# Kernel optimization log

Hardware: AMD Instinct MI355X
Metric: run time of the kernel (lower is better)

The kernel has to match this reference:

```python
import jax, jax.numpy as jnp
import numpy as np
from jax import lax

NEG_INF = -jnp.inf

def _conv_same(x, w, b):
    # x: [B,C,H,W], w: [O,C,5,5], padding=2 (SAME for k=5)
    y = lax.conv_general_dilated(x, w, (1, 1), [(2, 2), (2, 2)],
                                 dimension_numbers=('NCHW', 'OIHW', 'NCHW'))
    return y + b[None, :, None, None]

def _maxpool3(x):
    # kernel=3, stride=3, VALID: 28x28 -> 9x9
    return lax.reduce_window(x, -jnp.inf, lax.max, (1, 1, 3, 3), (1, 1, 3, 3), 'VALID')

def _trunk(x, w1, b1, w2, b2):
    # x: [B,1,28,28] -> [B, 16*9*9]
    h = jax.nn.relu(_conv_same(x, w1, b1))
    h = jax.nn.relu(_conv_same(h, w2, b2))
    h = _maxpool3(h)
    return h.reshape(h.shape[0], -1)

def _iterator(state, c_w1, c_b1, c_w2, c_b2, c_wl, c_bl):
    # state: [B,28,28]
    B = state.shape[0]
    xd = state[:, None]                                   # [B,1,28,28]
    feat = _trunk(xd, c_w1, c_b1, c_w2, c_b2)             # [B,1296]
    w = jnp.tanh(feat @ c_wl + c_bl).reshape(B, 1, 13, 13)  # per-sample kernels [O=B,I=1,13,13]
    xp = jnp.pad(xd, ((0, 0), (0, 0), (6, 6), (6, 6)), constant_values=-1.0)  # [B,1,40,40]
    xg = xp.reshape(1, B, 40, 40)
    yg = lax.conv_general_dilated(xg, w, (1, 1), 'VALID',
                                  feature_group_count=B,
                                  dimension_numbers=('NCHW', 'OIHW', 'NCHW'))  # [1,B,28,28]
    return yg.reshape(B, 28, 28)

def setup_inputs() -> dict:
    key = jax.random.key(0)
    ks = jax.random.split(key, 13)
    s = 0.05
    B = 1024
    inp = {
        'x': jax.random.normal(ks[0], (B, 28, 28), jnp.float32),
        # determine_n params
        'n_w1': jax.random.normal(ks[1], (8, 1, 5, 5), jnp.float32) * s,
        'n_b1': jnp.zeros((8,), jnp.float32),
        'n_w2': jax.random.normal(ks[2], (16, 8, 5, 5), jnp.float32) * s,
        'n_b2': jnp.zeros((16,), jnp.float32),
        'n_wl': jax.random.normal(ks[3], (16 * 9 * 9, 10), jnp.float32) * s,
        'n_bl': jnp.zeros((10,), jnp.float32),
        # determine_conv params
        'c_w1': jax.random.normal(ks[4], (8, 1, 5, 5), jnp.float32) * s,
        'c_b1': jnp.zeros((8,), jnp.float32),
        'c_w2': jax.random.normal(ks[5], (16, 8, 5, 5), jnp.float32) * s,
        'c_b2': jnp.zeros((16,), jnp.float32),
        'c_wl': jax.random.normal(ks[6], (16 * 9 * 9, 13 * 13), jnp.float32) * s,
        'c_bl': jnp.zeros((13 * 13,), jnp.float32),
    }
    return inp

def reference(x, n_w1, n_b1, n_w2, n_b2, n_wl, n_bl,
              c_w1, c_b1, c_w2, c_b2, c_wl, c_bl):
    B = x.shape[0]
    xd = x.reshape(B, 1, 28, 28)
    # determine_n: soft natural number over {0..9}
    num = jnp.tanh(_trunk(xd, n_w1, n_b1, n_w2, n_b2) @ n_wl + n_bl)  # [B,10]
    # TmIter: weighted sum of iterates r_0..r_9, r_{k+1} = iterator(r_k)
    r = x
    out = num[:, 0, None, None] * r
    for k in range(1, 10):  # fixed 9-step unroll (num encodes naturals 0..9)
        r = _iterator(r, c_w1, c_b1, c_w2, c_b2, c_wl, c_bl)
        out = out + num[:, k, None, None] * r
    return out.reshape(-1, 28, 28)
```

## Files before the change

### kernel.cpp

```cpp
#include <hip/hip_runtime.h>
#include <math.h>

#define RP40S 44
#define H1W   31

struct SharedBufs {
    float rp40[40*RP40S];
    float h1p[8*28*H1W];
    float pbuf[1296];
    float wker[169];
    float num_s[10];
    int   next;
};

template<int OUT>
__device__ __forceinline__ void fc_tanh(const float* __restrict__ Wg,
                                        const float* __restrict__ bg,
                                        const float* __restrict__ p,
                                        float* __restrict__ dst, int tid)
{
    if (tid < OUT) {
        float a[8];
        #pragma unroll
        for (int u = 0; u < 8; ++u) a[u] = 0.f;
        #pragma unroll 4
        for (int i0 = 0; i0 < 1296; i0 += 8) {
            #pragma unroll
            for (int u = 0; u < 8; ++u)
                a[u] = fmaf(p[i0+u], Wg[(i0+u)*OUT + tid], a[u]);
        }
        float s = ((a[0]+a[1])+(a[2]+a[3])) + ((a[4]+a[5])+(a[6]+a[7])) + bg[tid];
        dst[tid] = tanhf(s);
    }
}

#define C2_LOADROW(dst, YY) {                                                  \
    int rr_ = crow0 + (YY); rr_ = rr_ < 2 ? 2 : (rr_ > 29 ? 29 : rr_);         \
    const float* hp_ = plane + (rr_ - 2)*H1W;                                  \
    _Pragma("unroll") for (int j = 0; j < 13; ++j) dst[j] = hp_[j]; }

#define C2_FMAROW(src, YY)                                                     \
    if ((unsigned)(crow0 + (YY) - 2) <= 27u) {                                 \
      _Pragma("unroll") for (int t = 0; t < 3; ++t) {                          \
        const int ky_ = (YY) - t;                                              \
        if (ky_ >= 0 && ky_ <= 4) {                                            \
          _Pragma("unroll") for (int kx = 0; kx < 5; ++kx) {                   \
            const float w_ = wreg[ky_*5+kx];                                   \
            _Pragma("unroll") for (int u = 0; u < 9; ++u)                      \
              acc[t*9+u] = fmaf(w_, src[u+kx], acc[t*9+u]); } } } }

__device__ __forceinline__ void trunk_pass(SharedBufs& sb, int tid,
                                           const float* __restrict__ w1g,
                                           const float* __restrict__ b1g,
                                           const float* __restrict__ w2g,
                                           const float* __restrict__ b2g)
{
    if (tid < 224) {
        const int c = tid & 7;
        const int y = tid >> 3;
        float wreg[25];
        #pragma unroll
        for (int t = 0; t < 25; ++t) wreg[t] = w1g[c*25 + t];
        float csR[5];
        float S_all = 0.f, SR = 0.f;
        #pragma unroll
        for (int kx = 0; kx < 5; ++kx) {
            float a = wreg[kx] + wreg[5+kx] + wreg[10+kx] + wreg[15+kx] + wreg[20+kx];
            float ex = 0.f;
            if (y == 0)       ex = wreg[kx] + wreg[5+kx];
            else if (y == 1)  ex = wreg[kx];
            if (y == 26)      ex += wreg[20+kx];
            else if (y == 27) ex += wreg[15+kx] + wreg[20+kx];
            csR[kx] = a - ex;
            S_all += a; SR += csR[kx];
        }
        const float corrI = S_all - SR;
        const float bias  = b1g[c];
        float acc[28];
        #pragma unroll
        for (int x = 0; x < 28; ++x) acc[x] = bias + corrI;
        acc[0]  += csR[0] + csR[1];
        acc[1]  += csR[0];
        acc[26] += csR[4];
        acc[27] += csR[3] + csR[4];
        #pragma unroll
        for (int ky = 0; ky < 5; ++ky) {
            const float4* rr = (const float4*)&sb.rp40[(y+4+ky)*RP40S + 4];
            float rv[32];
            #pragma unroll
            for (int q = 0; q < 8; ++q) {
                float4 t = rr[q];
                rv[q*4+0]=t.x; rv[q*4+1]=t.y; rv[q*4+2]=t.z; rv[q*4+3]=t.w;
            }
            #pragma unroll
            for (int kx = 0; kx < 5; ++kx) {
                const float w = wreg[ky*5+kx];
                #pragma unroll
                for (int x = 0; x < 28; ++x) acc[x] = fmaf(w, rv[x+kx], acc[x]);
            }
        }
        float* hp = &sb.h1p[(c*28 + y)*H1W + 2];
        #pragma unroll
        for (int x = 0; x < 28; ++x) hp[x] = fmaxf(acc[x], 0.f);
    }
    __syncthreads();

    if (tid < 240) {
        const int c    = tid / 15;
        const int rem  = tid % 15;
        const int pyg  = rem / 3;
        const int pxg  = rem % 3;
        const int col0 = pxg * 9;
        const float bias = b2g[c];
        #pragma unroll 1
        for (int h = 0; h < 2; ++h) {
            const int py = pyg*2 + h;
            if (py >= 9) break;
            const int crow0 = py * 3;
            float acc[27];
            #pragma unroll
            for (int i = 0; i < 27; ++i) acc[i] = bias;
            for (int ic = 0; ic < 8; ++ic) {
                float wreg[25];
                const float* wsrc = &w2g[(c*8+ic)*25];
                #pragma unroll
                for (int t = 0; t < 25; ++t) wreg[t] = wsrc[t];
                const float* plane = &sb.h1p[ic*28*H1W + col0];
                float ra[13], rb[13];
                C2_LOADROW(ra, 0)
                C2_LOADROW(rb, 1)  C2_FMAROW(ra, 0)
                C2_LOADROW(ra, 2)  C2_FMAROW(rb, 1)
                C2_LOADROW(rb, 3)  C2_FMAROW(ra, 2)
                C2_LOADROW(ra, 4)  C2_FMAROW(rb, 3)
                C2_LOADROW(rb, 5)  C2_FMAROW(ra, 4)
                C2_LOADROW(ra, 6)  C2_FMAROW(rb, 5)
                                   C2_FMAROW(ra, 6)
            }
            #pragma unroll
            for (int pxi = 0; pxi < 3; ++pxi) {
                float m = acc[pxi*3];
                #pragma unroll
                for (int dy = 0; dy < 3; ++dy)
                    #pragma unroll
                    for (int dx = 0; dx < 3; ++dx)
                        m = fmaxf(m, acc[dy*9 + pxi*3 + dx]);
                sb.pbuf[c*81 + py*9 + pxg*3 + pxi] = fmaxf(m, 0.f);
            }
        }
    }
    __syncthreads();
}

__device__ __forceinline__ void depthwise13_regs(SharedBufs& sb, int y, int x0,
                                                 float& a0, float& a1,
                                                 float& a2, float& a3)
{
    a0=0.f; a1=0.f; a2=0.f; a3=0.f;
    #pragma unroll 1
    for (int ky = 0; ky < 13; ++ky) {
        const float4* rr = (const float4*)&sb.rp40[(y+ky)*RP40S + x0];
        float rv[16];
        #pragma unroll
        for (int q = 0; q < 4; ++q) {
            float4 t = rr[q];
            rv[q*4+0]=t.x; rv[q*4+1]=t.y; rv[q*4+2]=t.z; rv[q*4+3]=t.w;
        }
        const float* wr = &sb.wker[ky*13];
        #pragma unroll
        for (int kx = 0; kx < 13; ++kx) {
            const float w = wr[kx];
            a0 = fmaf(w, rv[kx+0], a0);
            a1 = fmaf(w, rv[kx+1], a1);
            a2 = fmaf(w, rv[kx+2], a2);
            a3 = fmaf(w, rv[kx+3], a3);
        }
    }
}

__global__ __launch_bounds__(256) __attribute__((amdgpu_num_vgpr(128)))
void modeld_fused(const float* __restrict__ x,
                  const float* __restrict__ n_w1, const float* __restrict__ n_b1,
                  const float* __restrict__ n_w2, const float* __restrict__ n_b2,
                  const float* __restrict__ n_wl, const float* __restrict__ n_bl,
                  const float* __restrict__ c_w1, const float* __restrict__ c_b1,
                  const float* __restrict__ c_w2, const float* __restrict__ c_b2,
                  const float* __restrict__ c_wl, const float* __restrict__ c_bl,
                  float* __restrict__ out,
                  int* __restrict__ counter, int B)
{
    __shared__ SharedBufs sb;
    const int tid = threadIdx.x;
    const int dy  = tid / 7;
    const int dx0 = (tid % 7) * 4;

    for (int i = tid; i < 40*RP40S;   i += 256) sb.rp40[i] = -1.f;
    for (int i = tid; i < 8*28*H1W;   i += 256) sb.h1p[i]  = 0.f;

    while (true) {
        if (tid == 0) sb.next = atomicAdd(counter, 1);
        __syncthreads();
        const int b = sb.next;
        if (b >= B) break;

        float cur[4] = {0.f, 0.f, 0.f, 0.f};
        if (tid < 196) {
            const float4 t = *(const float4*)&x[b*784 + dy*28 + dx0];
            cur[0]=t.x; cur[1]=t.y; cur[2]=t.z; cur[3]=t.w;
            float* rp = &sb.rp40[(dy+6)*RP40S + dx0 + 6];
            rp[0]=t.x; rp[1]=t.y; rp[2]=t.z; rp[3]=t.w;
        }
        __syncthreads();

        trunk_pass(sb, tid, n_w1, n_b1, n_w2, n_b2);
        fc_tanh<10>(n_wl, n_bl, sb.pbuf, sb.num_s, tid);
        __syncthreads();

        float o[4];
        {
            const float n0 = sb.num_s[0];
            #pragma unroll
            for (int q = 0; q < 4; ++q) o[q] = n0 * cur[q];
        }

        for (int k = 1; k <= 9; ++k) {
            trunk_pass(sb, tid, c_w1, c_b1, c_w2, c_b2);
            fc_tanh<169>(c_wl, c_bl, sb.pbuf, sb.wker, tid);
            __syncthreads();
            float a0, a1, a2, a3;
            if (tid < 196) depthwise13_regs(sb, dy, dx0, a0, a1, a2, a3);
            __syncthreads();
            if (tid < 196) {
                const float nk = sb.num_s[k];
                o[0] = fmaf(nk, a0, o[0]);
                o[1] = fmaf(nk, a1, o[1]);
                o[2] = fmaf(nk, a2, o[2]);
                o[3] = fmaf(nk, a3, o[3]);
                float* rp = &sb.rp40[(dy+6)*RP40S + dx0 + 6];
                rp[0]=a0; rp[1]=a1; rp[2]=a2; rp[3]=a3;
            }
            __syncthreads();
        }

        if (tid < 196)
            *(float4*)&out[b*784 + dy*28 + dx0] = make_float4(o[0], o[1], o[2], o[3]);
    }
}

extern "C" void kernel_launch(void* const* d_in, const int* in_sizes, int n_in,
                              void* d_out, int out_size, void* d_ws, size_t ws_size,
                              hipStream_t stream)
{
    const float* x    = (const float*)d_in[0];
    const float* n_w1 = (const float*)d_in[1];
    const float* n_b1 = (const float*)d_in[2];
    const float* n_w2 = (const float*)d_in[3];
    const float* n_b2 = (const float*)d_in[4];
    const float* n_wl = (const float*)d_in[5];
    const float* n_bl = (const float*)d_in[6];
    const float* c_w1 = (const float*)d_in[7];
    const float* c_b1 = (const float*)d_in[8];
    const float* c_w2 = (const float*)d_in[9];
    const float* c_b2 = (const float*)d_in[10];
    const float* c_wl = (const float*)d_in[11];
    const float* c_bl = (const float*)d_in[12];
    float* out = (float*)d_out;

    const int B = in_sizes[0] / 784;
    hipMemsetAsync(d_ws, 0, sizeof(int), stream);
    const int grid = B < 1024 ? B : 1024;
    hipLaunchKernelGGL(modeld_fused, dim3(grid), dim3(256), 0, stream,
                       x, n_w1, n_b1, n_w2, n_b2, n_wl, n_bl,
                       c_w1, c_b1, c_w2, c_b2, c_wl, c_bl, out,
                       (int*)d_ws, B);
}
```

Measured before the change: 1.342 ms.

## Register-block conv2 over channel pairs and vectorize shared-memory loads

Conv2 is reorganized so each thread computes two output channels for one pooled row, reusing each loaded input row for both channels. That replaces the earlier loop where each thread handled two pooled rows of one channel. The h1p stride is widened to allow float2 stores and loads, and the FC layer reads features as float4. The VGPR budget is raised to 168, which lowers occupancy, and the persistent grid is cut to 768 blocks to match.

```diff
diff --git a/kernel.cpp b/kernel.cpp
--- a/kernel.cpp
+++ b/kernel.cpp
@@ -2,7 +2,7 @@
 #include <math.h>
 
 #define RP40S 44
-#define H1W   31
+#define H1W   34
 
 struct SharedBufs {
     float rp40[40*RP40S];
@@ -25,29 +25,21 @@
         for (int u = 0; u < 8; ++u) a[u] = 0.f;
         #pragma unroll 4
         for (int i0 = 0; i0 < 1296; i0 += 8) {
-            #pragma unroll
-            for (int u = 0; u < 8; ++u)
-                a[u] = fmaf(p[i0+u], Wg[(i0+u)*OUT + tid], a[u]);
+            const float4 p0 = *(const float4*)&p[i0];
+            const float4 p1 = *(const float4*)&p[i0+4];
+            a[0] = fmaf(p0.x, Wg[(i0+0)*OUT + tid], a[0]);
+            a[1] = fmaf(p0.y, Wg[(i0+1)*OUT + tid], a[1]);
+            a[2] = fmaf(p0.z, Wg[(i0+2)*OUT + tid], a[2]);
+            a[3] = fmaf(p0.w, Wg[(i0+3)*OUT + tid], a[3]);
+            a[4] = fmaf(p1.x, Wg[(i0+4)*OUT + tid], a[4]);
+            a[5] = fmaf(p1.y, Wg[(i0+5)*OUT + tid], a[5]);
+            a[6] = fmaf(p1.z, Wg[(i0+6)*OUT + tid], a[6]);
+            a[7] = fmaf(p1.w, Wg[(i0+7)*OUT + tid], a[7]);
         }
         float s = ((a[0]+a[1])+(a[2]+a[3])) + ((a[4]+a[5])+(a[6]+a[7])) + bg[tid];
         dst[tid] = tanhf(s);
     }
 }
-
-#define C2_LOADROW(dst, YY) {                                                  \
-    int rr_ = crow0 + (YY); rr_ = rr_ < 2 ? 2 : (rr_ > 29 ? 29 : rr_);         \
-    const float* hp_ = plane + (rr_ - 2)*H1W;                                  \
-    _Pragma("unroll") for (int j = 0; j < 13; ++j) dst[j] = hp_[j]; }
-
-#define C2_FMAROW(src, YY)                                                     \
-    if ((unsigned)(crow0 + (YY) - 2) <= 27u) {                                 \
-      _Pragma("unroll") for (int t = 0; t < 3; ++t) {                          \
-        const int ky_ = (YY) - t;                                              \
-        if (ky_ >= 0 && ky_ <= 4) {                                            \
-          _Pragma("unroll") for (int kx = 0; kx < 5; ++kx) {                   \
-            const float w_ = wreg[ky_*5+kx];                                   \
-            _Pragma("unroll") for (int u = 0; u < 9; ++u)                      \
-              acc[t*9+u] = fmaf(w_, src[u+kx], acc[t*9+u]); } } } }
 
 __device__ __forceinline__ void trunk_pass(SharedBufs& sb, int tid,
                                            const float* __restrict__ w1g,
@@ -99,52 +91,83 @@
                 for (int x = 0; x < 28; ++x) acc[x] = fmaf(w, rv[x+kx], acc[x]);
             }
         }
-        float* hp = &sb.h1p[(c*28 + y)*H1W + 2];
-        #pragma unroll
-        for (int x = 0; x < 28; ++x) hp[x] = fmaxf(acc[x], 0.f);
+        float2* hp = (float2*)&sb.h1p[(c*28 + y)*H1W + 2];
+        #pragma unroll
+        for (int x = 0; x < 14; ++x)
+            hp[x] = make_float2(fmaxf(acc[2*x], 0.f), fmaxf(acc[2*x+1], 0.f));
     }
     __syncthreads();
 
     if (tid < 240) {
-        const int c    = tid / 15;
-        const int rem  = tid % 15;
-        const int pyg  = rem / 3;
-        const int pxg  = rem % 3;
-        const int col0 = pxg * 9;
-        const float bias = b2g[c];
-        #pragma unroll 1
-        for (int h = 0; h < 2; ++h) {
-            const int py = pyg*2 + h;
-            if (py >= 9) break;
+        const int cpair = tid / 30;
+        const int sp    = tid % 30;
+        const int h     = sp / 15;
+        const int rem   = sp % 15;
+        const int pyg   = rem / 3;
+        const int pxg   = rem % 3;
+        const int py    = pyg*2 + h;
+        if (py < 9) {
+            const int cA = cpair*2, cB = cA + 1;
+            const int colw = (pxg*9) & ~1;
+            const bool oddc = (pxg == 1);
             const int crow0 = py * 3;
-            float acc[27];
-            #pragma unroll
-            for (int i = 0; i < 27; ++i) acc[i] = bias;
+            float accA[27], accB[27];
+            {
+                const float bA = b2g[cA], bB = b2g[cB];
+                #pragma unroll
+                for (int i = 0; i < 27; ++i) { accA[i] = bA; accB[i] = bB; }
+            }
             for (int ic = 0; ic < 8; ++ic) {
-                float wreg[25];
-                const float* wsrc = &w2g[(c*8+ic)*25];
-                #pragma unroll
-                for (int t = 0; t < 25; ++t) wreg[t] = wsrc[t];
-                const float* plane = &sb.h1p[ic*28*H1W + col0];
-                float ra[13], rb[13];
-                C2_LOADROW(ra, 0)
-                C2_LOADROW(rb, 1)  C2_FMAROW(ra, 0)
-                C2_LOADROW(ra, 2)  C2_FMAROW(rb, 1)
-                C2_LOADROW(rb, 3)  C2_FMAROW(ra, 2)
-                C2_LOADROW(ra, 4)  C2_FMAROW(rb, 3)
-                C2_LOADROW(rb, 5)  C2_FMAROW(ra, 4)
-                C2_LOADROW(ra, 6)  C2_FMAROW(rb, 5)
-                                   C2_FMAROW(ra, 6)
+                float wA[25], wB[25];
+                {
+                    const float* sA = &w2g[(cA*8+ic)*25];
+                    const float* sB = &w2g[(cB*8+ic)*25];
+                    #pragma unroll
+                    for (int t = 0; t < 25; ++t) { wA[t] = sA[t]; wB[t] = sB[t]; }
+                }
+                #pragma unroll
+                for (int yy = 0; yy < 7; ++yy) {
+                    const int rr = crow0 + yy;
+                    if ((unsigned)(rr - 2) > 27u) continue;
+                    const float2* h2 = (const float2*)&sb.h1p[(ic*28 + (rr-2))*H1W + colw];
+                    float f[14];
+                    #pragma unroll
+                    for (int q = 0; q < 7; ++q) {
+                        float2 t = h2[q];
+                        f[2*q] = t.x; f[2*q+1] = t.y;
+                    }
+                    float rowv[13];
+                    #pragma unroll
+                    for (int j = 0; j < 13; ++j) rowv[j] = oddc ? f[j+1] : f[j];
+                    #pragma unroll
+                    for (int t = 0; t < 3; ++t) {
+                        const int ky = yy - t;
+                        if (ky < 0 || ky > 4) continue;
+                        #pragma unroll
+                        for (int kx = 0; kx < 5; ++kx) {
+                            const float wa = wA[ky*5+kx];
+                            const float wb = wB[ky*5+kx];
+                            #pragma unroll
+                            for (int u = 0; u < 9; ++u) {
+                                accA[t*9+u] = fmaf(wa, rowv[u+kx], accA[t*9+u]);
+                                accB[t*9+u] = fmaf(wb, rowv[u+kx], accB[t*9+u]);
+                            }
+                        }
+                    }
+                }
             }
             #pragma unroll
             for (int pxi = 0; pxi < 3; ++pxi) {
-                float m = acc[pxi*3];
+                float mA = accA[pxi*3], mB = accB[pxi*3];
                 #pragma unroll
                 for (int dy = 0; dy < 3; ++dy)
                     #pragma unroll
-                    for (int dx = 0; dx < 3; ++dx)
-                        m = fmaxf(m, acc[dy*9 + pxi*3 + dx]);
-                sb.pbuf[c*81 + py*9 + pxg*3 + pxi] = fmaxf(m, 0.f);
+                    for (int dx = 0; dx < 3; ++dx) {
+                        mA = fmaxf(mA, accA[dy*9 + pxi*3 + dx]);
+                        mB = fmaxf(mB, accB[dy*9 + pxi*3 + dx]);
+                    }
+                sb.pbuf[cA*81 + py*9 + pxg*3 + pxi] = fmaxf(mA, 0.f);
+                sb.pbuf[cB*81 + py*9 + pxg*3 + pxi] = fmaxf(mB, 0.f);
             }
         }
     }
@@ -177,7 +200,7 @@
     }
 }
 
-__global__ __launch_bounds__(256) __attribute__((amdgpu_num_vgpr(128)))
+__global__ __launch_bounds__(256) __attribute__((amdgpu_num_vgpr(168)))
 void modeld_fused(const float* __restrict__ x,
                   const float* __restrict__ n_w1, const float* __restrict__ n_b1,
                   const float* __restrict__ n_w2, const float* __restrict__ n_b2,
@@ -267,7 +290,7 @@
 
     const int B = in_sizes[0] / 784;
     hipMemsetAsync(d_ws, 0, sizeof(int), stream);
-    const int grid = B < 1024 ? B : 1024;
+    const int grid = B < 768 ? B : 768;
     hipLaunchKernelGGL(modeld_fused, dim3(grid), dim3(256), 0, stream,
                        x, n_w1, n_b1, n_w2, n_b2, n_wl, n_bl,
                        c_w1, c_b1, c_w2, c_b2, c_wl, c_bl, out,
```

After: 2.513 ms. 87.2% more time.

## Double-buffer iterate state to drop a barrier; vectorize FC loads, retune VGPRs and grid

Applied to the files above, without the earlier changes.

Splits the padded state buffer into two ping-pong copies, so the depthwise conv reads the current buffer and writes the next. This removes one __syncthreads per iteration. The FC loop now reads its pooled features as float4, the VGPR cap rises from 128 to 168, and the persistent grid shrinks from 1024 to 768 blocks. The larger shared footprint and register budget may lower occupancy, which the smaller grid partly anticipates.

```diff
diff --git a/kernel.cpp b/kernel.cpp
--- a/kernel.cpp
+++ b/kernel.cpp
@@ -5,7 +5,7 @@
 #define H1W   31
 
 struct SharedBufs {
-    float rp40[40*RP40S];
+    float rp40[2][40*RP40S];
     float h1p[8*28*H1W];
     float pbuf[1296];
     float wker[169];
@@ -25,9 +25,16 @@
         for (int u = 0; u < 8; ++u) a[u] = 0.f;
         #pragma unroll 4
         for (int i0 = 0; i0 < 1296; i0 += 8) {
-            #pragma unroll
-            for (int u = 0; u < 8; ++u)
-                a[u] = fmaf(p[i0+u], Wg[(i0+u)*OUT + tid], a[u]);
+            const float4 p0 = *(const float4*)&p[i0];
+            const float4 p1 = *(const float4*)&p[i0+4];
+            a[0] = fmaf(p0.x, Wg[(i0+0)*OUT + tid], a[0]);
+            a[1] = fmaf(p0.y, Wg[(i0+1)*OUT + tid], a[1]);
+            a[2] = fmaf(p0.z, Wg[(i0+2)*OUT + tid], a[2]);
+            a[3] = fmaf(p0.w, Wg[(i0+3)*OUT + tid], a[3]);
+            a[4] = fmaf(p1.x, Wg[(i0+4)*OUT + tid], a[4]);
+            a[5] = fmaf(p1.y, Wg[(i0+5)*OUT + tid], a[5]);
+            a[6] = fmaf(p1.z, Wg[(i0+6)*OUT + tid], a[6]);
+            a[7] = fmaf(p1.w, Wg[(i0+7)*OUT + tid], a[7]);
         }
         float s = ((a[0]+a[1])+(a[2]+a[3])) + ((a[4]+a[5])+(a[6]+a[7])) + bg[tid];
         dst[tid] = tanhf(s);
@@ -49,7 +56,9 @@
             _Pragma("unroll") for (int u = 0; u < 9; ++u)                      \
               acc[t*9+u] = fmaf(w_, src[u+kx], acc[t*9+u]); } } } }
 
-__device__ __forceinline__ void trunk_pass(SharedBufs& sb, int tid,
+__device__ __forceinline__ void trunk_pass(SharedBufs& sb,
+                                           const float* __restrict__ rpc,
+                                           int tid,
                                            const float* __restrict__ w1g,
                                            const float* __restrict__ b1g,
                                            const float* __restrict__ w2g,
@@ -85,7 +94,7 @@
         acc[27] += csR[3] + csR[4];
         #pragma unroll
         for (int ky = 0; ky < 5; ++ky) {
-            const float4* rr = (const float4*)&sb.rp40[(y+4+ky)*RP40S + 4];
+            const float4* rr = (const float4*)&rpc[(y+4+ky)*RP40S + 4];
             float rv[32];
             #pragma unroll
             for (int q = 0; q < 8; ++q) {
@@ -151,14 +160,16 @@
     __syncthreads();
 }
 
-__device__ __forceinline__ void depthwise13_regs(SharedBufs& sb, int y, int x0,
+__device__ __forceinline__ void depthwise13_regs(SharedBufs& sb,
+                                                 const float* __restrict__ rpc,
+                                                 int y, int x0,
                                                  float& a0, float& a1,
                                                  float& a2, float& a3)
 {
     a0=0.f; a1=0.f; a2=0.f; a3=0.f;
     #pragma unroll 1
     for (int ky = 0; ky < 13; ++ky) {
-        const float4* rr = (const float4*)&sb.rp40[(y+ky)*RP40S + x0];
+        const float4* rr = (const float4*)&rpc[(y+ky)*RP40S + x0];
         float rv[16];
         #pragma unroll
         for (int q = 0; q < 4; ++q) {
@@ -177,7 +188,7 @@
     }
 }
 
-__global__ __launch_bounds__(256) __attribute__((amdgpu_num_vgpr(128)))
+__global__ __launch_bounds__(256) __attribute__((amdgpu_num_vgpr(168)))
 void modeld_fused(const float* __restrict__ x,
                   const float* __restrict__ n_w1, const float* __restrict__ n_b1,
                   const float* __restrict__ n_w2, const float* __restrict__ n_b2,
@@ -193,7 +204,7 @@
     const int dy  = tid / 7;
     const int dx0 = (tid % 7) * 4;
 
-    for (int i = tid; i < 40*RP40S;   i += 256) sb.rp40[i] = -1.f;
+    for (int i = tid; i < 2*40*RP40S; i += 256) sb.rp40[0][i] = -1.f;
     for (int i = tid; i < 8*28*H1W;   i += 256) sb.h1p[i]  = 0.f;
 
     while (true) {
@@ -206,12 +217,12 @@
         if (tid < 196) {
             const float4 t = *(const float4*)&x[b*784 + dy*28 + dx0];
             cur[0]=t.x; cur[1]=t.y; cur[2]=t.z; cur[3]=t.w;
-            float* rp = &sb.rp40[(dy+6)*RP40S + dx0 + 6];
+            float* rp = &sb.rp40[0][(dy+6)*RP40S + dx0 + 6];
             rp[0]=t.x; rp[1]=t.y; rp[2]=t.z; rp[3]=t.w;
         }
         __syncthreads();
 
-        trunk_pass(sb, tid, n_w1, n_b1, n_w2, n_b2);
+        trunk_pass(sb, sb.rp40[0], tid, n_w1, n_b1, n_w2, n_b2);
         fc_tanh<10>(n_wl, n_bl, sb.pbuf, sb.num_s, tid);
         __syncthreads();
 
@@ -222,23 +233,26 @@
             for (int q = 0; q < 4; ++q) o[q] = n0 * cur[q];
         }
 
+        int curbuf = 0;
         for (int k = 1; k <= 9; ++k) {
-            trunk_pass(sb, tid, c_w1, c_b1, c_w2, c_b2);
+            const float* rpc = sb.rp40[curbuf];
+            float*       rpn = sb.rp40[curbuf ^ 1];
+            trunk_pass(sb, rpc, tid, c_w1, c_b1, c_w2, c_b2);
             fc_tanh<169>(c_wl, c_bl, sb.pbuf, sb.wker, tid);
             __syncthreads();
-            float a0, a1, a2, a3;
-            if (tid < 196) depthwise13_regs(sb, dy, dx0, a0, a1, a2, a3);
-            __syncthreads();
             if (tid < 196) {
+                float a0, a1, a2, a3;
+                depthwise13_regs(sb, rpc, dy, dx0, a0, a1, a2, a3);
                 const float nk = sb.num_s[k];
                 o[0] = fmaf(nk, a0, o[0]);
                 o[1] = fmaf(nk, a1, o[1]);
                 o[2] = fmaf(nk, a2, o[2]);
                 o[3] = fmaf(nk, a3, o[3]);
-                float* rp = &sb.rp40[(dy+6)*RP40S + dx0 + 6];
+                float* rp = &rpn[(dy+6)*RP40S + dx0 + 6];
                 rp[0]=a0; rp[1]=a1; rp[2]=a2; rp[3]=a3;
             }
             __syncthreads();
+            curbuf ^= 1;
         }
 
         if (tid < 196)
@@ -267,7 +281,7 @@
 
     const int B = in_sizes[0] / 784;
     hipMemsetAsync(d_ws, 0, sizeof(int), stream);
-    const int grid = B < 1024 ? B : 1024;
+    const int grid = B < 768 ? B : 768;
     hipLaunchKernelGGL(modeld_fused, dim3(grid), dim3(256), 0, stream,
                        x, n_w1, n_b1, n_w2, n_b2, n_wl, n_bl,
                        c_w1, c_b1, c_w2, c_b2, c_wl, c_bl, out,
```

After: 1.335 ms. Within noise of the previous version (-0.5%).
